# Optimization experiments

Hardware: AMD Instinct MI355X
Metric: run time of the kernel (lower is better)

## Reference

```python
import jax, jax.numpy as jnp
import numpy as np

D_MODEL = 1024
NUM_HEADS = 16
MAX_SEQ_LEN = 2048
THETA = 10000.0
HEAD_DIM = D_MODEL // NUM_HEADS  # 64


def _trunc_normal(key, shape, std):
    # truncated normal in [-3, 3] sigma, matching nn.init.trunc_normal_
    return std * jax.random.truncated_normal(key, -3.0, 3.0, shape, dtype=jnp.float32)


def setup_inputs() -> dict:
    key = jax.random.key(0)
    kx, kq, kk, kv, ko = jax.random.split(key, 5)
    B, L = 2, 2048
    sigma = np.sqrt(2.0 / (D_MODEL + D_MODEL))
    x = jax.random.normal(kx, (B, L, D_MODEL), dtype=jnp.float32)
    token_positions = jnp.arange(L, dtype=jnp.int64 if jax.config.jax_enable_x64 else jnp.int32)[None, :]
    return {
        "x": x,
        "wq": _trunc_normal(kq, (D_MODEL, D_MODEL), sigma),
        "wk": _trunc_normal(kk, (D_MODEL, D_MODEL), sigma),
        "wv": _trunc_normal(kv, (D_MODEL, D_MODEL), sigma),
        "wo": _trunc_normal(ko, (D_MODEL, D_MODEL), sigma),
        "token_positions": token_positions,
    }


def _rope_tables():
    pos = jnp.arange(MAX_SEQ_LEN, dtype=jnp.float32)
    d_idx = jnp.arange(HEAD_DIM // 2, dtype=jnp.float32)
    inv_freq = THETA ** (-2.0 * d_idx / HEAD_DIM)
    angles = pos[:, None] * inv_freq[None, :]  # [max_seq_len, head_dim/2]
    return jnp.cos(angles), jnp.sin(angles)


def _apply_rope(x, cos, sin):
    # x: [b, n, l, h]; cos/sin: [1, l, h/2] (broadcast over b, n)
    xe = x[..., 0::2]
    xo = x[..., 1::2]
    oe = cos * xe - sin * xo
    oo = sin * xe + cos * xo
    # interleave back: stack last axis then flatten pairs
    out = jnp.stack([oe, oo], axis=-1)
    return out.reshape(x.shape)


def reference(x, wq, wk, wv, wo, token_positions):
    B, L, _ = x.shape
    cos_t, sin_t = _rope_tables()
    cos = cos_t[token_positions]  # [1, L, h/2]
    sin = sin_t[token_positions]

    def proj(w):
        y = jnp.einsum('bld,ed->ble', x, w)
        return y.reshape(B, L, NUM_HEADS, HEAD_DIM).transpose(0, 2, 1, 3)  # b n l h

    q, k, v = proj(wq), proj(wk), proj(wv)
    q = _apply_rope(q, cos, sin)
    k = _apply_rope(k, cos, sin)

    scale = 1.0 / np.sqrt(HEAD_DIM).astype(np.float32)
    logits = jnp.einsum('bnqh,bnkh->bnqk', q, k) * scale
    causal = jnp.tril(jnp.ones((L, L), dtype=bool))
    logits = jnp.where(causal[None, None], logits, -jnp.inf)
    scores = jax.nn.softmax(logits, axis=-1)
    out = jnp.einsum('bnqk,bnkh->bnqh', scores, v)
    out = out.transpose(0, 2, 1, 3).reshape(B, L, D_MODEL)
    return jnp.einsum('bld,ed->ble', out, wo)
```

## Files before the change

kernel.cpp:

```cpp
#include <hip/hip_runtime.h>
#include <stdint.h>
#include <stddef.h>

#define SEQ   2048
#define HD    64
#define DM    1024
#define NHEAD 16

typedef __bf16 bf16x8 __attribute__((ext_vector_type(8)));
typedef __bf16 bf16x4 __attribute__((ext_vector_type(4)));
typedef float  f32x4  __attribute__((ext_vector_type(4)));

#define MFMA16x16(a, b, c) __builtin_amdgcn_mfma_f32_16x16x32_bf16((a), (b), (c), 0, 0, 0)

__device__ __forceinline__ void gload16(const void* g, void* lds_uniform) {
    __builtin_amdgcn_global_load_lds(
        (const __attribute__((address_space(1))) uint32_t*)g,
        (__attribute__((address_space(3))) uint32_t*)lds_uniform, 16, 0, 0);
}

__global__ void cvt_kernel(const float* __restrict__ in, __bf16* __restrict__ out, int n) {
    int i = (blockIdx.x * blockDim.x + threadIdx.x) * 4;
    if (i >= n) return;
    const float4 v = *(const float4*)(in + i);
    __bf16 o[4] = {(__bf16)v.x, (__bf16)v.y, (__bf16)v.z, (__bf16)v.w};
    *(uint64_t*)(out + i) = *(const uint64_t*)o;
}

__global__ void cvt4_kernel(const float* __restrict__ wq, const float* __restrict__ wk,
                            const float* __restrict__ wv, const float* __restrict__ wo,
                            __bf16* __restrict__ wqkv, __bf16* __restrict__ wob) {
    int g = blockIdx.x >> 10;
    int i = ((blockIdx.x & 1023) * 256 + threadIdx.x) * 4;
    const float* src = (g == 0) ? wq : (g == 1) ? wk : (g == 2) ? wv : wo;
    __bf16* dst = (g == 3) ? wob : (wqkv + (size_t)g * 1048576);
    const float4 v = *(const float4*)(src + i);
    __bf16 o[4] = {(__bf16)v.x, (__bf16)v.y, (__bf16)v.z, (__bf16)v.w};
    *(uint64_t*)(dst + i) = *(const uint64_t*)o;
}

__global__ void rope_tab_kernel(float* __restrict__ ct, float* __restrict__ st) {
    int i = blockIdx.x * blockDim.x + threadIdx.x;
    int p = i & 31;
    int pos = i >> 5;
    float freq = expf(-(float)p * (logf(10000.0f) / 32.0f));
    float ang = (float)pos * freq;
    ct[i] = cosf(ang);
    st[i] = sinf(ang);
}

template <int MODE>
__global__ __launch_bounds__(256, 2)
void gemm_bt_kernel(const __bf16* __restrict__ A, const __bf16* __restrict__ W,
                    float* __restrict__ C, __bf16* __restrict__ Qb,
                    __bf16* __restrict__ Kb, __bf16* __restrict__ VTb,
                    const int* __restrict__ tpos, const float* __restrict__ ct,
                    const float* __restrict__ st, int N, int K) {
    __shared__ __align__(16) char smem[32768];
    char* As = smem;
    char* Bs = smem + 16384;
    const int lane = threadIdx.x & 63;
    const int w    = threadIdx.x >> 6;
    const int bn = blockIdx.x, bm = blockIdx.y;
    const int rbase = (w >> 1) * 64;
    const int cbase = (w & 1) * 64;

    f32x4 acc[4][4] = {};

    const int kt_iters = K >> 6;
    for (int kt = 0; kt < kt_iters; ++kt) {
        #pragma unroll
        for (int c = 0; c < 4; ++c) {
            int id = (c * 4 + w) * 64 + lane;
            int row = id >> 3, cc = id & 7;
            int koff = kt * 64 + ((cc ^ (row & 7)) << 3);
            gload16(A + (size_t)(bm * 128 + row) * K + koff, As + (c * 4 + w) * 1024);
            gload16(W + (size_t)(bn * 128 + row) * K + koff, Bs + (c * 4 + w) * 1024);
        }
        __syncthreads();
        #pragma unroll
        for (int ks = 0; ks < 2; ++ks) {
            bf16x8 af[4], bfr[4];
            #pragma unroll
            for (int i = 0; i < 4; ++i) {
                int row = rbase + i * 16 + (lane & 15);
                int c = ks * 4 + (lane >> 4);
                af[i] = *(const bf16x8*)(As + row * 128 + ((c ^ (row & 7)) << 4));
            }
            #pragma unroll
            for (int j = 0; j < 4; ++j) {
                int row = cbase + j * 16 + (lane & 15);
                int c = ks * 4 + (lane >> 4);
                bfr[j] = *(const bf16x8*)(Bs + row * 128 + ((c ^ (row & 7)) << 4));
            }
            #pragma unroll
            for (int i = 0; i < 4; ++i)
                #pragma unroll
                for (int j = 0; j < 4; ++j)
                    acc[i][j] = MFMA16x16(af[i], bfr[j], acc[i][j]);
        }
        __syncthreads();
    }

    if (MODE == 1) {
        #pragma unroll
        for (int i = 0; i < 4; ++i)
            #pragma unroll
            for (int j = 0; j < 4; ++j)
                #pragma unroll
                for (int r = 0; r < 4; ++r) {
                    int m = bm * 128 + rbase + i * 16 + (lane >> 4) * 4 + r;
                    int n = bn * 128 + cbase + j * 16 + (lane & 15);
                    C[(size_t)m * N + n] = acc[i][j][r];
                }
    } else {
        const int which = bn >> 3;
        char* T = smem + w * 8192;
        #pragma unroll
        for (int i = 0; i < 4; ++i)
            #pragma unroll
            for (int j = 0; j < 4; ++j)
                #pragma unroll
                for (int r = 0; r < 4; ++r) {
                    int mi = i * 16 + (lane >> 4) * 4 + r;
                    int ni = j * 16 + (lane & 15);
                    __bf16 v = (__bf16)acc[i][j][r];
                    if (which == 2)
                        *(__bf16*)(T + ni * 128 + ((mi * 2) ^ ((ni & 7) << 4))) = v;
                    else
                        *(__bf16*)(T + mi * 128 + ((ni * 2) ^ ((mi & 7) << 4))) = v;
                }
        #pragma unroll
        for (int it = 0; it < 8; ++it) {
            int id = it * 64 + lane;
            int row = id >> 3, cc = id & 7;
            bf16x8 v = *(const bf16x8*)(T + row * 128 + ((cc ^ (row & 7)) << 4));
            if (which == 2) {
                int n = bn * 128 + cbase + row;
                int m = bm * 128 + rbase + cc * 8;
                int b = m >> 11, l = m & (SEQ - 1);
                int h = (n & (DM - 1)) >> 6, d = n & 63;
                *(bf16x8*)(VTb + ((size_t)((b * NHEAD + h) * HD + d) * SEQ) + l) = v;
            } else {
                int m = bm * 128 + rbase + row;
                int n = bn * 128 + cbase + cc * 8;
                int b = m >> 11, l = m & (SEQ - 1);
                int h = (n & (DM - 1)) >> 6, d = n & 63;
                int pb = tpos[l] * 32 + (d >> 1);
                float sc = (which == 0) ? 0.18033688011112042f : 1.0f;
                bf16x8 ov;
                #pragma unroll
                for (int jj = 0; jj < 4; ++jj) {
                    float cs = ct[pb + jj], sn = st[pb + jj];
                    float e = (float)v[2 * jj], dd = (float)v[2 * jj + 1];
                    ov[2 * jj]     = (__bf16)(sc * (cs * e - sn * dd));
                    ov[2 * jj + 1] = (__bf16)(sc * (sn * e + cs * dd));
                }
                __bf16* dst = which ? Kb : Qb;
                *(bf16x8*)(dst + ((size_t)(b * NHEAD + h) * SEQ + l) * HD + d) = ov;
            }
        }
    }
}

__global__ __launch_bounds__(256, 4)
void attn_kernel(const __bf16* __restrict__ Q, const __bf16* __restrict__ K,
                 const __bf16* __restrict__ VT, __bf16* __restrict__ O) {
    __shared__ __align__(16) char smem[40960];
    const int lane = threadIdx.x & 63;
    const int w    = threadIdx.x >> 6;
    const int tid  = threadIdx.x;
    char* Ps = smem + 32768 + w * 2048;

    const int bid = blockIdx.x;
    const int xcd = bid & 7;
    const int idx = bid >> 3;
    const int bh  = xcd * 4 + (idx & 3);
    const int qb  = 31 - (idx >> 2);

    const __bf16* Qbh  = Q  + (size_t)bh * SEQ * HD;
    const __bf16* Kbh  = K  + (size_t)bh * SEQ * HD;
    const __bf16* VTbh = VT + (size_t)bh * HD * SEQ;
    const int b = bh >> 4, h = bh & 15;

    #pragma unroll
    for (int c = 0; c < 2; ++c) {
        int id = (c * 4 + w) * 64 + lane;
        int row = id >> 3, cc = id & 7;
        int sw = (cc ^ (row & 7)) << 3;
        gload16(Kbh + (size_t)row * HD + sw, smem + (c * 4 + w) * 1024);
        gload16(VTbh + (size_t)row * SEQ + sw, smem + 8192 + (c * 4 + w) * 1024);
    }

    const int qrow = qb * 64 + w * 16 + (lane & 15);
    bf16x8 qf[2];
    qf[0] = *(const bf16x8*)(Qbh + (size_t)qrow * HD + (lane >> 4) * 8);
    qf[1] = *(const bf16x8*)(Qbh + (size_t)qrow * HD + 32 + (lane >> 4) * 8);

    f32x4 o[4] = {};
    float mrow = -1e30f;
    float lrow = 0.f;

    int cur = 0;
    __syncthreads();

    for (int kb = 0; kb <= qb; ++kb) {
        bf16x8 kreg[2], vreg[2];
        if (kb < qb) {
            #pragma unroll
            for (int c = 0; c < 2; ++c) {
                int id = c * 256 + tid;
                int row = id >> 3, cc = id & 7;
                kreg[c] = *(const bf16x8*)(Kbh + (size_t)((kb + 1) * 64 + row) * HD + cc * 8);
                vreg[c] = *(const bf16x8*)(VTbh + (size_t)row * SEQ + (kb + 1) * 64 + cc * 8);
            }
        }

        char* Ks = smem + cur * 16384;
        char* Vs = Ks + 8192;

        f32x4 s[4];
        #pragma unroll
        for (int jt = 0; jt < 4; ++jt) {
            f32x4 z = {};
            #pragma unroll
            for (int ks = 0; ks < 2; ++ks) {
                int row = jt * 16 + (lane & 15);
                int c = ks * 4 + (lane >> 4);
                bf16x8 kf = *(const bf16x8*)(Ks + row * 128 + ((c ^ (row & 7)) << 4));
                z = MFMA16x16(kf, qf[ks], z);
            }
            s[jt] = z;
        }

        if (kb == qb) {
            int i = qb * 64 + w * 16 + (lane & 15);
            #pragma unroll
            for (int jt = 0; jt < 4; ++jt)
                #pragma unroll
                for (int r = 0; r < 4; ++r) {
                    int j = kb * 64 + jt * 16 + (lane >> 4) * 4 + r;
                    if (j > i) s[jt][r] = -1e30f;
                }
        }

        float pmax = fmaxf(fmaxf(fmaxf(s[0][0], s[0][1]), fmaxf(s[0][2], s[0][3])),
                           fmaxf(fmaxf(s[1][0], s[1][1]), fmaxf(s[1][2], s[1][3])));
        pmax = fmaxf(pmax,
               fmaxf(fmaxf(fmaxf(s[2][0], s[2][1]), fmaxf(s[2][2], s[2][3])),
                     fmaxf(fmaxf(s[3][0], s[3][1]), fmaxf(s[3][2], s[3][3]))));

        if (!__all(pmax <= mrow + 8.0f)) {
            pmax = fmaxf(pmax, __shfl_xor(pmax, 16));
            pmax = fmaxf(pmax, __shfl_xor(pmax, 32));
            float mn = fmaxf(mrow, pmax);
            float alpha = exp2f(mrow - mn);
            mrow = mn;
            lrow *= alpha;
            float ar[4];
            #pragma unroll
            for (int r = 0; r < 4; ++r) ar[r] = __shfl(alpha, (lane >> 4) * 4 + r);
            #pragma unroll
            for (int dt = 0; dt < 4; ++dt)
                #pragma unroll
                for (int r = 0; r < 4; ++r)
                    o[dt][r] *= ar[r];
        }

        {
            int qr = lane & 15;
            int swrow = (qr & 7) << 4;
            float rs = 0.f;
            #pragma unroll
            for (int jt = 0; jt < 4; ++jt) {
                bf16x4 pk;
                #pragma unroll
                for (int r = 0; r < 4; ++r) {
                    float pv = exp2f(s[jt][r] - mrow);
                    rs += pv;
                    pk[r] = (__bf16)pv;
                }
                int jj = (jt * 16 + (lane >> 4) * 4) * 2;
                *(bf16x4*)(Ps + qr * 128 + (jj ^ swrow)) = pk;
            }
            lrow += rs;
        }

        #pragma unroll
        for (int js = 0; js < 2; ++js) {
            int prow = lane & 15;
            int cb = js * 4 + (lane >> 4);
            bf16x8 pf = *(const bf16x8*)(Ps + prow * 128 + ((cb ^ (prow & 7)) << 4));
            #pragma unroll
            for (int dt = 0; dt < 4; ++dt) {
                int vrow = dt * 16 + (lane & 15);
                bf16x8 vf = *(const bf16x8*)(Vs + vrow * 128 + ((cb ^ (vrow & 7)) << 4));
                o[dt] = MFMA16x16(pf, vf, o[dt]);
            }
        }

        if (kb < qb) {
            char* Kn = smem + (cur ^ 1) * 16384;
            char* Vn = Kn + 8192;
            #pragma unroll
            for (int c = 0; c < 2; ++c) {
                int id = c * 256 + tid;
                int row = id >> 3, cc = id & 7;
                int sw = (cc ^ (row & 7)) << 4;
                *(bf16x8*)(Kn + row * 128 + sw) = kreg[c];
                *(bf16x8*)(Vn + row * 128 + sw) = vreg[c];
            }
        }
        __syncthreads();
        cur ^= 1;
    }

    lrow += __shfl_xor(lrow, 16);
    lrow += __shfl_xor(lrow, 32);
    float linv[4];
    #pragma unroll
    for (int r = 0; r < 4; ++r) {
        float lr = __shfl(lrow, (lane >> 4) * 4 + r);
        linv[r] = 1.0f / lr;
    }

    char* Os = smem + 32768;
    #pragma unroll
    for (int dt = 0; dt < 4; ++dt)
        #pragma unroll
        for (int r = 0; r < 4; ++r) {
            int orow = w * 16 + (lane >> 4) * 4 + r;
            int oc = (dt * 16 + (lane & 15)) * 2;
            *(__bf16*)(Os + orow * 128 + (oc ^ ((orow & 7) << 4))) = (__bf16)(o[dt][r] * linv[r]);
        }
    __syncthreads();

    #pragma unroll
    for (int c = 0; c < 2; ++c) {
        int id = c * 256 + tid;
        int row = id >> 3, cc = id & 7;
        bf16x8 v = *(const bf16x8*)(Os + row * 128 + ((cc ^ (row & 7)) << 4));
        *(bf16x8*)(O + (size_t)(b * SEQ + qb * 64 + row) * DM + h * HD + cc * 8) = v;
    }
}

extern "C" void kernel_launch(void* const* d_in, const int* in_sizes, int n_in,
                              void* d_out, int out_size, void* d_ws, size_t ws_size,
                              hipStream_t stream) {
    const float* x  = (const float*)d_in[0];
    const float* wq = (const float*)d_in[1];
    const float* wk = (const float*)d_in[2];
    const float* wv = (const float*)d_in[3];
    const float* wo = (const float*)d_in[4];
    const int* tpos = (const int*)d_in[5];
    float* out = (float*)d_out;
    char* ws = (char*)d_ws;

    __bf16* xb   = (__bf16*)(ws);
    __bf16* wqkv = (__bf16*)(ws + (size_t)(8  << 20));
    __bf16* wob  = (__bf16*)(ws + (size_t)(14 << 20));
    __bf16* Qb   = (__bf16*)(ws + (size_t)(16 << 20));
    __bf16* Kb   = (__bf16*)(ws + (size_t)(24 << 20));
    __bf16* VTb  = (__bf16*)(ws + (size_t)(32 << 20));
    __bf16* Ob   = (__bf16*)(ws + (size_t)(40 << 20));
    float* ct    = (float*)(ws + (size_t)(48 << 20));
    float* st    = (float*)(ws + (size_t)(48 << 20) + 262144);

    cvt_kernel<<<4096, 256, 0, stream>>>(x, xb, 4194304);
    cvt4_kernel<<<4096, 256, 0, stream>>>(wq, wk, wv, wo, wqkv, wob);
    rope_tab_kernel<<<256, 256, 0, stream>>>(ct, st);
    gemm_bt_kernel<0><<<dim3(24, 32), 256, 0, stream>>>(xb, wqkv, nullptr, Qb, Kb, VTb,
                                                        tpos, ct, st, 3072, 1024);
    attn_kernel<<<1024, 256, 0, stream>>>(Qb, Kb, VTb, Ob);
    gemm_bt_kernel<1><<<dim3(8, 32), 256, 0, stream>>>(Ob, wob, out, nullptr, nullptr, nullptr,
                                                       nullptr, nullptr, nullptr, 1024, 1024);
}
```

Measured before the change: 115.9 us.

## Merge prep kernels into one launch and remap GEMM blocks per XCD

```diff
diff --git a/kernel.cpp b/kernel.cpp
--- a/kernel.cpp
+++ b/kernel.cpp
@@ -19,38 +19,39 @@
         (__attribute__((address_space(3))) uint32_t*)lds_uniform, 16, 0, 0);
 }
 
-__global__ void cvt_kernel(const float* __restrict__ in, __bf16* __restrict__ out, int n) {
-    int i = (blockIdx.x * blockDim.x + threadIdx.x) * 4;
-    if (i >= n) return;
-    const float4 v = *(const float4*)(in + i);
-    __bf16 o[4] = {(__bf16)v.x, (__bf16)v.y, (__bf16)v.z, (__bf16)v.w};
-    *(uint64_t*)(out + i) = *(const uint64_t*)o;
-}
-
-__global__ void cvt4_kernel(const float* __restrict__ wq, const float* __restrict__ wk,
+__global__ void prep_kernel(const float* __restrict__ x,
+                            const float* __restrict__ wq, const float* __restrict__ wk,
                             const float* __restrict__ wv, const float* __restrict__ wo,
-                            __bf16* __restrict__ wqkv, __bf16* __restrict__ wob) {
-    int g = blockIdx.x >> 10;
-    int i = ((blockIdx.x & 1023) * 256 + threadIdx.x) * 4;
-    const float* src = (g == 0) ? wq : (g == 1) ? wk : (g == 2) ? wv : wo;
-    __bf16* dst = (g == 3) ? wob : (wqkv + (size_t)g * 1048576);
-    const float4 v = *(const float4*)(src + i);
-    __bf16 o[4] = {(__bf16)v.x, (__bf16)v.y, (__bf16)v.z, (__bf16)v.w};
-    *(uint64_t*)(dst + i) = *(const uint64_t*)o;
-}
-
-__global__ void rope_tab_kernel(float* __restrict__ ct, float* __restrict__ st) {
-    int i = blockIdx.x * blockDim.x + threadIdx.x;
-    int p = i & 31;
-    int pos = i >> 5;
-    float freq = expf(-(float)p * (logf(10000.0f) / 32.0f));
-    float ang = (float)pos * freq;
-    ct[i] = cosf(ang);
-    st[i] = sinf(ang);
+                            __bf16* __restrict__ xb, __bf16* __restrict__ wqkv,
+                            __bf16* __restrict__ wob,
+                            float* __restrict__ ct, float* __restrict__ st) {
+    int bid = blockIdx.x;
+    if (bid < 4096) {
+        int i = (bid * 256 + threadIdx.x) * 4;
+        const float4 v = *(const float4*)(x + i);
+        __bf16 o[4] = {(__bf16)v.x, (__bf16)v.y, (__bf16)v.z, (__bf16)v.w};
+        *(uint64_t*)(xb + i) = *(const uint64_t*)o;
+    } else if (bid < 8192) {
+        int g = (bid - 4096) >> 10;
+        int i = (((bid - 4096) & 1023) * 256 + threadIdx.x) * 4;
+        const float* src = (g == 0) ? wq : (g == 1) ? wk : (g == 2) ? wv : wo;
+        __bf16* dst = (g == 3) ? wob : (wqkv + (size_t)g * 1048576);
+        const float4 v = *(const float4*)(src + i);
+        __bf16 o[4] = {(__bf16)v.x, (__bf16)v.y, (__bf16)v.z, (__bf16)v.w};
+        *(uint64_t*)(dst + i) = *(const uint64_t*)o;
+    } else {
+        int i = (bid - 8192) * 256 + threadIdx.x;
+        int p = i & 31;
+        int pos = i >> 5;
+        float freq = expf(-(float)p * (logf(10000.0f) / 32.0f));
+        float ang = (float)pos * freq;
+        ct[i] = cosf(ang);
+        st[i] = sinf(ang);
+    }
 }
 
 template <int MODE>
-__global__ __launch_bounds__(256, 2)
+__global__ __launch_bounds__(256, 3)
 void gemm_bt_kernel(const __bf16* __restrict__ A, const __bf16* __restrict__ W,
                     float* __restrict__ C, __bf16* __restrict__ Qb,
                     __bf16* __restrict__ Kb, __bf16* __restrict__ VTb,
@@ -61,7 +62,14 @@
     char* Bs = smem + 16384;
     const int lane = threadIdx.x & 63;
     const int w    = threadIdx.x >> 6;
-    const int bn = blockIdx.x, bm = blockIdx.y;
+
+    const int nbn = N >> 7;
+    const int per = (nbn * 32) >> 3;
+    const int id  = blockIdx.x;
+    const int lin = (id & 7) * per + (id >> 3);
+    const int bm  = lin / nbn;
+    const int bn  = lin % nbn;
+
     const int rbase = (w >> 1) * 64;
     const int cbase = (w & 1) * 64;
 
@@ -71,8 +79,8 @@
     for (int kt = 0; kt < kt_iters; ++kt) {
         #pragma unroll
         for (int c = 0; c < 4; ++c) {
-            int id = (c * 4 + w) * 64 + lane;
-            int row = id >> 3, cc = id & 7;
+            int id2 = (c * 4 + w) * 64 + lane;
+            int row = id2 >> 3, cc = id2 & 7;
             int koff = kt * 64 + ((cc ^ (row & 7)) << 3);
             gload16(A + (size_t)(bm * 128 + row) * K + koff, As + (c * 4 + w) * 1024);
             gload16(W + (size_t)(bn * 128 + row) * K + koff, Bs + (c * 4 + w) * 1024);
@@ -132,8 +140,8 @@
                 }
         #pragma unroll
         for (int it = 0; it < 8; ++it) {
-            int id = it * 64 + lane;
-            int row = id >> 3, cc = id & 7;
+            int id2 = it * 64 + lane;
+            int row = id2 >> 3, cc = id2 & 7;
             bf16x8 v = *(const bf16x8*)(T + row * 128 + ((cc ^ (row & 7)) << 4));
             if (which == 2) {
                 int n = bn * 128 + cbase + row;
@@ -366,12 +374,10 @@
     float* ct    = (float*)(ws + (size_t)(48 << 20));
     float* st    = (float*)(ws + (size_t)(48 << 20) + 262144);
 
-    cvt_kernel<<<4096, 256, 0, stream>>>(x, xb, 4194304);
-    cvt4_kernel<<<4096, 256, 0, stream>>>(wq, wk, wv, wo, wqkv, wob);
-    rope_tab_kernel<<<256, 256, 0, stream>>>(ct, st);
-    gemm_bt_kernel<0><<<dim3(24, 32), 256, 0, stream>>>(xb, wqkv, nullptr, Qb, Kb, VTb,
-                                                        tpos, ct, st, 3072, 1024);
+    prep_kernel<<<8448, 256, 0, stream>>>(x, wq, wk, wv, wo, xb, wqkv, wob, ct, st);
+    gemm_bt_kernel<0><<<768, 256, 0, stream>>>(xb, wqkv, nullptr, Qb, Kb, VTb,
+                                               tpos, ct, st, 3072, 1024);
     attn_kernel<<<1024, 256, 0, stream>>>(Qb, Kb, VTb, Ob);
-    gemm_bt_kernel<1><<<dim3(8, 32), 256, 0, stream>>>(Ob, wob, out, nullptr, nullptr, nullptr,
-                                                       nullptr, nullptr, nullptr, 1024, 1024);
-}
+    gemm_bt_kernel<1><<<256, 256, 0, stream>>>(Ob, wob, out, nullptr, nullptr, nullptr,
+                                               nullptr, nullptr, nullptr, 1024, 1024);
+}
```

New measurement: 108.5 us. 6.4% less time.
